# Performance work log

Measured on AMD Instinct MI355X. Metric: run time of the kernel, lower is better.

The kernel has to match this reference:

```python
import jax, jax.numpy as jnp
import numpy as np

KNOTS = 8
INTERVAL = 4.0
LAYERS = 8
WIDTH = 128
DX = 64
DY = 64
P = 3 * KNOTS - 1  # widths(K) + heights(K) + interior derivatives(K-1)
BATCH = 16384
MIN_DERIV = 1e-3
SOFTMAX_ADJ = 1e-2


def _made_masks(D, W):
    in_deg = np.arange(1, D + 1)
    hid_deg = (np.arange(W) % max(D - 1, 1)) + 1
    m1 = (hid_deg[:, None] >= in_deg[None, :]).astype(np.float32)        # (W, D)
    out_deg = np.repeat(np.arange(1, D + 1), P)                           # (D*P,)
    m2 = (out_deg[:, None] > hid_deg[None, :]).astype(np.float32)        # (D*P, W)
    return jnp.asarray(m1), jnp.asarray(m2)


def _adj_softmax(v):
    p = jax.nn.softmax(v, axis=-1)
    return (p + SOFTMAX_ADJ / v.shape[-1]) / (1.0 + SOFTMAX_ADJ)


def _rqs_transform(x, params):
    # x: (B, D); params: (B, D, P). Rational-quadratic spline on [-B_int, B_int], identity outside.
    Bi = INTERVAL
    w = params[..., :KNOTS]
    h = params[..., KNOTS:2 * KNOTS]
    d = params[..., 2 * KNOTS:]
    widths = _adj_softmax(w) * 2 * Bi
    heights = _adj_softmax(h) * 2 * Bi
    zero = jnp.zeros(x.shape + (1,), x.dtype)
    x_pos = -Bi + jnp.concatenate([zero, jnp.cumsum(widths, -1)], -1)   # (B, D, K+1)
    y_pos = -Bi + jnp.concatenate([zero, jnp.cumsum(heights, -1)], -1)
    derivs = jax.nn.softplus(d) + MIN_DERIV                              # (B, D, K-1)
    one = jnp.ones(x.shape + (1,), x.dtype)
    derivs = jnp.concatenate([one, derivs, one], -1)                     # (B, D, K+1), boundary derivs = 1
    inside = (x > -Bi) & (x < Bi)
    xc = jnp.clip(x, -Bi, Bi)
    # bin search (K is small; vectorized comparison)
    k = jnp.clip(jnp.sum((xc[..., None] >= x_pos), -1) - 1, 0, KNOTS - 1)

    def g(a, i):
        return jnp.take_along_axis(a, i[..., None], -1)[..., 0]

    xk, xk1 = g(x_pos, k), g(x_pos, k + 1)
    yk, yk1 = g(y_pos, k), g(y_pos, k + 1)
    dk, dk1 = g(derivs, k), g(derivs, k + 1)
    sk = (yk1 - yk) / (xk1 - xk)
    xi = (xc - xk) / (xk1 - xk)
    omx = 1.0 - xi
    den = sk + (dk1 + dk - 2.0 * sk) * xi * omx
    out = yk + (yk1 - yk) * (sk * xi * xi + dk * xi * omx) / den
    ld = 2.0 * jnp.log(sk) + jnp.log(dk1 * xi * xi + 2.0 * sk * xi * omx + dk * omx * omx) - 2.0 * jnp.log(den)
    return jnp.where(inside, out, x), jnp.where(inside, ld, 0.0)


def _maf_transform(x, W1, b1, Wout, bout, D):
    # Stacked layers: masked MLP -> elementwise RQ spline -> reverse permutation.
    m1, m2 = _made_masks(D, WIDTH)

    def layer(carry, ws):
        xc, ld = carry
        w1, bb1, wo, bo = ws
        hdn = jax.nn.relu(xc @ (w1 * m1).T + bb1)                # (B, W)
        p = (hdn @ (wo * m2).T + bo).reshape(xc.shape[0], D, P)  # (B, D, P)
        x2, ldj = _rqs_transform(xc, p)
        return (x2[:, ::-1], ld + ldj.sum(-1)), None

    init = (x, jnp.zeros(x.shape[0], x.dtype))
    (xf, ld), _ = jax.lax.scan(layer, init, (W1, b1, Wout, bout))
    return xf, ld


def setup_inputs() -> dict:
    key = jax.random.key(0)
    ks = jax.random.split(key, 10)
    s = 0.05
    return {
        "x": jax.random.normal(ks[0], (BATCH, DX), jnp.float32),
        "y": jax.random.normal(ks[1], (BATCH, DY), jnp.float32),
        "f_W1": jax.random.normal(ks[2], (LAYERS, WIDTH, DX), jnp.float32) * s,
        "f_b1": jnp.zeros((LAYERS, WIDTH), jnp.float32),
        "f_Wout": jax.random.normal(ks[3], (LAYERS, DX * P, WIDTH), jnp.float32) * s,
        "f_bout": jnp.zeros((LAYERS, DX * P), jnp.float32),
        "g_W1": jax.random.normal(ks[4], (LAYERS, WIDTH, DY), jnp.float32) * s,
        "g_b1": jnp.zeros((LAYERS, WIDTH), jnp.float32),
        "g_Wout": jax.random.normal(ks[5], (LAYERS, DY * P, WIDTH), jnp.float32) * s,
        "g_bout": jnp.zeros((LAYERS, DY * P), jnp.float32),
    }


def reference(x, y, f_W1, f_b1, f_Wout, f_bout, g_W1, g_b1, g_Wout, g_bout):
    xo, ldf = _maf_transform(x, f_W1, f_b1, f_Wout, f_bout, DX)
    yo, ldg = _maf_transform(y, g_W1, g_b1, g_Wout, g_bout, DY)
    return (xo, ldf, yo, ldg)
```

## Files before the change

kernel.cpp:

```cpp
#include <hip/hip_runtime.h>
#include <math.h>

#define BATCH   16384
#define DIMS    64
#define WID     128
#define KN      8
#define NP      23
#define NCOL    (DIMS * NP)
#define NLAYERS 8
#define BI_F    4.0f
#define GRP     92
#define NGRPB   8
#define LOG2E   1.44269504f

#define PF_WOUT (NLAYERS * NCOL * WID)
#define PF_W1   (NLAYERS * WID * DIMS)

typedef short s16x8 __attribute__((ext_vector_type(8)));
typedef float f32x4 __attribute__((ext_vector_type(4)));

__device__ __forceinline__ unsigned short f2bf(float f) {
    unsigned int u = __builtin_bit_cast(unsigned int, f);
    unsigned int r = (u + 0x7FFFu + ((u >> 16) & 1u)) >> 16;
    return (unsigned short)r;
}
__device__ __forceinline__ float bf2f(unsigned short u) {
    return __builtin_bit_cast(float, (unsigned int)u << 16);
}

__device__ __forceinline__ void stage16(const unsigned short* g, unsigned short* l) {
    __builtin_amdgcn_global_load_lds(
        (__attribute__((address_space(1))) void*)g,
        (__attribute__((address_space(3))) void*)l,
        16, 0, 0);
}

__global__ __launch_bounds__(256) void premask_kernel(
    const float* __restrict__ f_wout, const float* __restrict__ g_wout,
    const float* __restrict__ f_w1,   const float* __restrict__ g_w1,
    unsigned short* __restrict__ womask, unsigned short* __restrict__ w1mask,
    float* __restrict__ ldf, float* __restrict__ ldg)
{
    const int idx    = blockIdx.x * 256 + threadIdx.x;
    const int stride = gridDim.x * 256;

    const int totw = 2 * PF_WOUT;
    for (int i = idx; i < totw; i += stride) {
        int fl = i / PF_WOUT;
        int r  = i % PF_WOUT;
        int h  = r % WID;
        int o  = (r / WID) % NCOL;
        int d  = o / NP;
        int hd = h % (DIMS - 1) + 1;
        const float* src = fl ? g_wout : f_wout;
        unsigned short v = (hd <= d) ? f2bf(src[r] * LOG2E) : (unsigned short)0;
        const int dst = i - h + (h ^ ((o & 7) << 4));
        womask[dst] = v;
    }

    const int tot1 = 2 * PF_W1;
    for (int i = idx; i < tot1; i += stride) {
        int fl = i / PF_W1;
        int r  = i % PF_W1;
        int c  = r % DIMS;
        int w  = (r / DIMS) % WID;
        int deg = w % (DIMS - 1) + 1;
        const float* src = fl ? g_w1 : f_w1;
        w1mask[i] = (c < deg) ? f2bf(src[r]) : (unsigned short)0;
    }

    for (int i = idx; i < BATCH; i += stride) {
        ldf[i] = 0.0f;
        ldg[i] = 0.0f;
    }
}

__global__ __launch_bounds__(256)
__attribute__((amdgpu_waves_per_eu(4, 4)))
void layer_kernel(
    const float* __restrict__ xin_f, const float* __restrict__ xin_g,
    float* __restrict__ xout_f,      float* __restrict__ xout_g,
    const unsigned short* __restrict__ w1m_f, const unsigned short* __restrict__ w1m_g,
    const float* __restrict__ b1_f,  const float* __restrict__ b1_g,
    const unsigned short* __restrict__ wom_f, const unsigned short* __restrict__ wom_g,
    const float* __restrict__ bo_f,  const float* __restrict__ bo_g,
    float* __restrict__ ld_f,        float* __restrict__ ld_g)
{
    __shared__ __align__(16) unsigned short Wl[GRP * WID];
    __shared__ __align__(16) unsigned short S[4][2176];

    const int t     = threadIdx.x;
    const int wv    = t >> 6;
    const int ln    = t & 63;
    const int m     = ln & 15;
    const int q     = ln >> 4;
    const int flow  = blockIdx.y & 1;
    const int dhalf = blockIdx.y >> 1;
    const int g0    = dhalf * NGRPB;
    const int r0    = blockIdx.x * 64 + wv * 16;

    const float* xin          = flow ? xin_g : xin_f;
    float*       xout         = flow ? xout_g : xout_f;
    const unsigned short* w1m = flow ? w1m_g : w1m_f;
    const float* b1           = flow ? b1_g  : b1_f;
    const unsigned short* wom = flow ? wom_g : wom_f;
    const float* bo           = flow ? bo_g  : bo_f;
    float*       ldp          = flow ? ld_g  : ld_f;

    {
        const unsigned short* src = wom + (size_t)g0 * GRP * WID + ln * 8;
        #pragma unroll
        for (int i = 0; i < 6; ++i) {
            const int c = wv + 4 * i;
            if (c < 23) stage16(src + c * 512, Wl + c * 512);
        }
    }

    const float* xrow = xin + (size_t)(r0 + m) * DIMS;
    s16x8 xa[2];
    #pragma unroll
    for (int ks = 0; ks < 2; ++ks) {
        float4 v0 = *(const float4*)(xrow + ks * 32 + q * 8);
        float4 v1 = *(const float4*)(xrow + ks * 32 + q * 8 + 4);
        s16x8 a;
        a[0] = (short)f2bf(v0.x); a[1] = (short)f2bf(v0.y);
        a[2] = (short)f2bf(v0.z); a[3] = (short)f2bf(v0.w);
        a[4] = (short)f2bf(v1.x); a[5] = (short)f2bf(v1.y);
        a[6] = (short)f2bf(v1.z); a[7] = (short)f2bf(v1.w);
        xa[ks] = a;
    }

    f32x4 hacc[8];
    #pragma unroll
    for (int nt = 0; nt < 8; ++nt) {
        float bv = b1[nt * 16 + m];
        hacc[nt] = (f32x4){bv, bv, bv, bv};
    }
    #pragma unroll
    for (int ks = 0; ks < 2; ++ks) {
        #pragma unroll
        for (int nt = 0; nt < 8; ++nt) {
            s16x8 bfr = *(const s16x8*)(w1m + (nt * 16 + m) * DIMS + ks * 32 + q * 8);
            hacc[nt] = __builtin_amdgcn_mfma_f32_16x16x32_bf16(xa[ks], bfr, hacc[nt], 0, 0, 0);
        }
    }
    unsigned short* sw = &S[wv][0];
    #pragma unroll
    for (int nt = 0; nt < 8; ++nt) {
        #pragma unroll
        for (int rr = 0; rr < 4; ++rr) {
            sw[(q * 4 + rr) * 136 + nt * 16 + m] = f2bf(fmaxf(hacc[nt][rr], 0.0f));
        }
    }
    asm volatile("" ::: "memory");

    s16x8 af[4];
    #pragma unroll
    for (int ks = 0; ks < 4; ++ks)
        af[ks] = *(const s16x8*)&sw[m * 136 + ks * 32 + q * 8];
    asm volatile("" ::: "memory");

    float bnx[6];
    #pragma unroll
    for (int nt = 0; nt < 6; ++nt) {
        int o = g0 * GRP + nt * 16 + m;
        o = (o < NCOL) ? o : (NCOL - 1);
        bnx[nt] = bo[o] * LOG2E;
    }
    float xcur = xin[(size_t)(r0 + m) * DIMS + g0 * 4 + q];
    float xnxt = 0.0f;

    float ldsum = 0.0f;

    __syncthreads();

    #pragma unroll 1
    for (int gl = 0; gl < NGRPB; ++gl) {
        const int gg = g0 + gl;

        f32x4 acc[6];
        #pragma unroll
        for (int nt = 0; nt < 6; ++nt)
            acc[nt] = (f32x4){bnx[nt], bnx[nt], bnx[nt], bnx[nt]};

        const int swz = ((gg * 4 + m) & 7) << 4;
        #pragma unroll
        for (int ks = 0; ks < 4; ++ks) {
            #pragma unroll
            for (int nt = 0; nt < 6; ++nt) {
                const s16x8 bfr = *(const s16x8*)&Wl[
                    (nt * 16 + m) * WID + ((ks * 32 + q * 8) ^ swz)];
                acc[nt] = __builtin_amdgcn_mfma_f32_16x16x32_bf16(af[ks], bfr, acc[nt], 0, 0, 0);
            }
        }

        if (gl < NGRPB - 1) {
            __syncthreads();
            const unsigned short* src = wom + (size_t)(gg + 1) * GRP * WID + ln * 8;
            #pragma unroll
            for (int i = 0; i < 6; ++i) {
                const int c = wv + 4 * i;
                if (c < 23) stage16(src + c * 512, Wl + c * 512);
            }
            #pragma unroll
            for (int nt = 0; nt < 6; ++nt) {
                int o = (gg + 1) * GRP + nt * 16 + m;
                o = (o < NCOL) ? o : (NCOL - 1);
                bnx[nt] = bo[o] * LOG2E;
            }
            xnxt = xin[(size_t)(r0 + m) * DIMS + (gg + 1) * 4 + q];
        }

        #pragma unroll
        for (int nt = 0; nt < 6; ++nt) {
            const int c18 = (nt * 16 + m) * 18 + q * 4;
            #pragma unroll
            for (int rr = 0; rr < 4; ++rr)
                sw[c18 + rr] = f2bf(acc[nt][rr]);
        }

        {
            const int d = gg * 4 + q;

            float pp[NP];
            #pragma unroll
            for (int j = 0; j < NP; ++j)
                pp[j] = bf2f(sw[(q * 23 + j) * 18 + m]);

            const float xraw = xcur;

            float ew[KN], eh[KN];
            #pragma unroll
            for (int j = 0; j < KN; ++j) {
                ew[j] = exp2f(pp[j]);
                eh[j] = exp2f(pp[8 + j]);
            }
            const float sw_ = ((ew[0] + ew[1]) + (ew[2] + ew[3]))
                            + ((ew[4] + ew[5]) + (ew[6] + ew[7]));
            const float sh_ = ((eh[0] + eh[1]) + (eh[2] + eh[3]))
                            + ((eh[4] + eh[5]) + (eh[6] + eh[7]));
            const float cmul = 8.0f / 1.01f;
            const float cadd = 0.00125f * (8.0f / 1.01f);
            const float rw = cmul / sw_, rh = cmul / sh_;
            float width[KN], height[KN];
            #pragma unroll
            for (int j = 0; j < KN; ++j) {
                width[j]  = fmaf(ew[j], rw, cadd);
                height[j] = fmaf(eh[j], rh, cadd);
            }
            float dv[KN + 1];
            dv[0] = 1.0f; dv[KN] = 1.0f;
            #pragma unroll
            for (int i = 1; i < KN; ++i) {
                const float tt = exp2f(pp[15 + i]);
                dv[i] = fmaf(__log2f(1.0f + tt), 0.69314718f, 0.001f);
            }

            const bool inside = (xraw > -BI_F) && (xraw < BI_F);
            const float xcl = fminf(fmaxf(xraw, -BI_F), BI_F);

            float cx = -BI_F, cy = -BI_F;
            float xk = -BI_F, yk = -BI_F, xk1 = 0.f, yk1 = 0.f, dk = 1.f, dk1 = 1.f;
            #pragma unroll
            for (int i = 0; i < KN; ++i) {
                const float nx = cx + width[i];
                const float ny = cy + height[i];
                const bool cc = (xcl >= cx);
                xk  = cc ? cx : xk;    yk  = cc ? cy : yk;
                xk1 = cc ? nx : xk1;   yk1 = cc ? ny : yk1;
                dk  = cc ? dv[i] : dk; dk1 = cc ? dv[i + 1] : dk1;
                cx = nx; cy = ny;
            }

            const float invw = 1.0f / (xk1 - xk);
            const float sk   = (yk1 - yk) * invw;
            const float xi   = (xcl - xk) * invw;
            const float omx  = 1.0f - xi;
            const float den  = sk + (dk1 + dk - 2.0f * sk) * xi * omx;
            const float rden = 1.0f / den;
            float outv = fmaf((yk1 - yk) * (sk * xi * xi + dk * xi * omx), rden, yk);
            const float numl = dk1 * xi * xi + 2.0f * sk * xi * omx + dk * omx * omx;
            float ldj = __logf(sk * sk * numl * rden * rden);
            outv = inside ? outv : xraw;
            ldj  = inside ? ldj : 0.0f;

            xout[(size_t)(r0 + m) * DIMS + (DIMS - 1 - d)] = outv;
            ldsum += ldj;
        }

        if (gl < NGRPB - 1) {
            __syncthreads();
            xcur = xnxt;
        }
    }

    float v = ldsum + __shfl_xor(ldsum, 16, 64);
    v = v + __shfl_xor(v, 32, 64);
    if (ln < 16) {
        atomicAdd(ldp + (r0 + ln), v);
    }
}

extern "C" void kernel_launch(void* const* d_in, const int* in_sizes, int n_in,
                              void* d_out, int out_size, void* d_ws, size_t ws_size,
                              hipStream_t stream)
{
    const float* x      = (const float*)d_in[0];
    const float* y      = (const float*)d_in[1];
    const float* f_W1   = (const float*)d_in[2];
    const float* f_b1   = (const float*)d_in[3];
    const float* f_Wout = (const float*)d_in[4];
    const float* f_bout = (const float*)d_in[5];
    const float* g_W1   = (const float*)d_in[6];
    const float* g_b1   = (const float*)d_in[7];
    const float* g_Wout = (const float*)d_in[8];
    const float* g_bout = (const float*)d_in[9];

    float* out = (float*)d_out;
    float* xo  = out;
    float* ldf = out + (size_t)BATCH * DIMS;
    float* yo  = ldf + BATCH;
    float* ldg = yo + (size_t)BATCH * DIMS;

    unsigned short* womask = (unsigned short*)d_ws;
    unsigned short* w1mask = womask + 2 * (size_t)PF_WOUT;
    float* xA_f = (float*)(w1mask + 2 * (size_t)PF_W1);
    float* xA_g = xA_f + (size_t)BATCH * DIMS;

    premask_kernel<<<dim3(2048), dim3(256), 0, stream>>>(
        f_Wout, g_Wout, f_W1, g_W1, womask, w1mask, ldf, ldg);

    for (int l = 0; l < NLAYERS; ++l) {
        const float* inf = (l == 0) ? x : ((l & 1) ? xA_f : xo);
        const float* ing = (l == 0) ? y : ((l & 1) ? xA_g : yo);
        float* outf = (l & 1) ? xo : xA_f;
        float* outg = (l & 1) ? yo : xA_g;

        layer_kernel<<<dim3(BATCH / 64, 4), dim3(256), 0, stream>>>(
            inf, ing, outf, outg,
            w1mask + (size_t)l * WID * DIMS,
            w1mask + (size_t)PF_W1 + (size_t)l * WID * DIMS,
            f_b1 + (size_t)l * WID, g_b1 + (size_t)l * WID,
            womask + (size_t)l * NCOL * WID,
            womask + (size_t)PF_WOUT + (size_t)l * NCOL * WID,
            f_bout + (size_t)l * NCOL, g_bout + (size_t)l * NCOL,
            ldf, ldg);
    }
}
```

Before: 469.3 us.

## Fuse all eight flow layers into one persistent kernel with LDS-resident activations

Replaces the eight per-layer launches with a single kernel in which each block processes 64 rows through all layers. Activations are kept in double-buffered LDS instead of round-tripping through global memory, and the log-det is written once rather than accumulated with atomics. The grid drops from a 4-way split of output groups to a 2-way split across the flows, and occupancy is lowered to 2 waves/EU, so each block now streams all Wout groups itself. This removes launch overhead and intermediate traffic but reduces parallelism, with 512 blocks and longer serial work per block.

```diff
diff --git a/kernel.cpp b/kernel.cpp
--- a/kernel.cpp
+++ b/kernel.cpp
@@ -10,7 +10,8 @@
 #define NLAYERS 8
 #define BI_F    4.0f
 #define GRP     92
-#define NGRPB   8
+#define NGRP    16
+#define XPITCH  68
 #define LOG2E   1.44269504f
 
 #define PF_WOUT (NLAYERS * NCOL * WID)
@@ -38,8 +39,7 @@
 __global__ __launch_bounds__(256) void premask_kernel(
     const float* __restrict__ f_wout, const float* __restrict__ g_wout,
     const float* __restrict__ f_w1,   const float* __restrict__ g_w1,
-    unsigned short* __restrict__ womask, unsigned short* __restrict__ w1mask,
-    float* __restrict__ ldf, float* __restrict__ ldg)
+    unsigned short* __restrict__ womask, unsigned short* __restrict__ w1mask)
 {
     const int idx    = blockIdx.x * 256 + threadIdx.x;
     const int stride = gridDim.x * 256;
@@ -68,16 +68,11 @@
         const float* src = fl ? g_w1 : f_w1;
         w1mask[i] = (c < deg) ? f2bf(src[r]) : (unsigned short)0;
     }
-
-    for (int i = idx; i < BATCH; i += stride) {
-        ldf[i] = 0.0f;
-        ldg[i] = 0.0f;
-    }
 }
 
 __global__ __launch_bounds__(256)
-__attribute__((amdgpu_waves_per_eu(4, 4)))
-void layer_kernel(
+__attribute__((amdgpu_waves_per_eu(2, 2)))
+void flow8_kernel(
     const float* __restrict__ xin_f, const float* __restrict__ xin_g,
     float* __restrict__ xout_f,      float* __restrict__ xout_g,
     const unsigned short* __restrict__ w1m_f, const unsigned short* __restrict__ w1m_g,
@@ -88,16 +83,15 @@
 {
     __shared__ __align__(16) unsigned short Wl[GRP * WID];
     __shared__ __align__(16) unsigned short S[4][2176];
-
-    const int t     = threadIdx.x;
-    const int wv    = t >> 6;
-    const int ln    = t & 63;
-    const int m     = ln & 15;
-    const int q     = ln >> 4;
-    const int flow  = blockIdx.y & 1;
-    const int dhalf = blockIdx.y >> 1;
-    const int g0    = dhalf * NGRPB;
-    const int r0    = blockIdx.x * 64 + wv * 16;
+    __shared__ __align__(16) float Xf[2][4][16][XPITCH];
+
+    const int t    = threadIdx.x;
+    const int wv   = t >> 6;
+    const int ln   = t & 63;
+    const int m    = ln & 15;
+    const int q    = ln >> 4;
+    const int flow = blockIdx.y;
+    const int r0   = blockIdx.x * 64 + wv * 16;
 
     const float* xin          = flow ? xin_g : xin_f;
     float*       xout         = flow ? xout_g : xout_f;
@@ -108,7 +102,18 @@
     float*       ldp          = flow ? ld_g  : ld_f;
 
     {
-        const unsigned short* src = wom + (size_t)g0 * GRP * WID + ln * 8;
+        const int row = ln >> 2;
+        const int c0  = (ln & 3) * 16;
+        const float* srcr = xin + (size_t)(r0 + row) * DIMS + c0;
+        float* dstr = &Xf[0][wv][row][c0];
+        #pragma unroll
+        for (int i = 0; i < 4; ++i)
+            *(float4*)(dstr + i * 4) = *(const float4*)(srcr + i * 4);
+    }
+    asm volatile("" ::: "memory");
+
+    {
+        const unsigned short* src = wom + ln * 8;
         #pragma unroll
         for (int i = 0; i < 6; ++i) {
             const int c = wv + 4 * i;
@@ -116,188 +121,205 @@
         }
     }
 
-    const float* xrow = xin + (size_t)(r0 + m) * DIMS;
-    s16x8 xa[2];
-    #pragma unroll
-    for (int ks = 0; ks < 2; ++ks) {
-        float4 v0 = *(const float4*)(xrow + ks * 32 + q * 8);
-        float4 v1 = *(const float4*)(xrow + ks * 32 + q * 8 + 4);
-        s16x8 a;
-        a[0] = (short)f2bf(v0.x); a[1] = (short)f2bf(v0.y);
-        a[2] = (short)f2bf(v0.z); a[3] = (short)f2bf(v0.w);
-        a[4] = (short)f2bf(v1.x); a[5] = (short)f2bf(v1.y);
-        a[6] = (short)f2bf(v1.z); a[7] = (short)f2bf(v1.w);
-        xa[ks] = a;
-    }
-
-    f32x4 hacc[8];
-    #pragma unroll
-    for (int nt = 0; nt < 8; ++nt) {
-        float bv = b1[nt * 16 + m];
-        hacc[nt] = (f32x4){bv, bv, bv, bv};
-    }
-    #pragma unroll
-    for (int ks = 0; ks < 2; ++ks) {
-        #pragma unroll
-        for (int nt = 0; nt < 8; ++nt) {
-            s16x8 bfr = *(const s16x8*)(w1m + (nt * 16 + m) * DIMS + ks * 32 + q * 8);
-            hacc[nt] = __builtin_amdgcn_mfma_f32_16x16x32_bf16(xa[ks], bfr, hacc[nt], 0, 0, 0);
-        }
-    }
-    unsigned short* sw = &S[wv][0];
-    #pragma unroll
-    for (int nt = 0; nt < 8; ++nt) {
-        #pragma unroll
-        for (int rr = 0; rr < 4; ++rr) {
-            sw[(q * 4 + rr) * 136 + nt * 16 + m] = f2bf(fmaxf(hacc[nt][rr], 0.0f));
-        }
-    }
-    asm volatile("" ::: "memory");
-
-    s16x8 af[4];
-    #pragma unroll
-    for (int ks = 0; ks < 4; ++ks)
-        af[ks] = *(const s16x8*)&sw[m * 136 + ks * 32 + q * 8];
-    asm volatile("" ::: "memory");
-
     float bnx[6];
     #pragma unroll
-    for (int nt = 0; nt < 6; ++nt) {
-        int o = g0 * GRP + nt * 16 + m;
-        o = (o < NCOL) ? o : (NCOL - 1);
-        bnx[nt] = bo[o] * LOG2E;
-    }
-    float xcur = xin[(size_t)(r0 + m) * DIMS + g0 * 4 + q];
-    float xnxt = 0.0f;
+    for (int nt = 0; nt < 6; ++nt)
+        bnx[nt] = bo[nt * 16 + m] * LOG2E;
 
     float ldsum = 0.0f;
+    int cur = 0;
+    unsigned short* sw = &S[wv][0];
 
     __syncthreads();
 
     #pragma unroll 1
-    for (int gl = 0; gl < NGRPB; ++gl) {
-        const int gg = g0 + gl;
-
-        f32x4 acc[6];
-        #pragma unroll
-        for (int nt = 0; nt < 6; ++nt)
-            acc[nt] = (f32x4){bnx[nt], bnx[nt], bnx[nt], bnx[nt]};
-
-        const int swz = ((gg * 4 + m) & 7) << 4;
-        #pragma unroll
-        for (int ks = 0; ks < 4; ++ks) {
+    for (int l = 0; l < NLAYERS; ++l) {
+        const unsigned short* w1m_l = w1m + (size_t)l * WID * DIMS;
+        const float* b1_l           = b1 + (size_t)l * WID;
+        const int nxt = cur ^ 1;
+
+        s16x8 xa[2];
+        #pragma unroll
+        for (int ks = 0; ks < 2; ++ks) {
+            float4 v0 = *(const float4*)&Xf[cur][wv][m][ks * 32 + q * 8];
+            float4 v1 = *(const float4*)&Xf[cur][wv][m][ks * 32 + q * 8 + 4];
+            s16x8 a;
+            a[0] = (short)f2bf(v0.x); a[1] = (short)f2bf(v0.y);
+            a[2] = (short)f2bf(v0.z); a[3] = (short)f2bf(v0.w);
+            a[4] = (short)f2bf(v1.x); a[5] = (short)f2bf(v1.y);
+            a[6] = (short)f2bf(v1.z); a[7] = (short)f2bf(v1.w);
+            xa[ks] = a;
+        }
+
+        f32x4 hacc[8];
+        #pragma unroll
+        for (int nt = 0; nt < 8; ++nt) {
+            float bv = b1_l[nt * 16 + m];
+            hacc[nt] = (f32x4){bv, bv, bv, bv};
+        }
+        #pragma unroll
+        for (int ks = 0; ks < 2; ++ks) {
+            #pragma unroll
+            for (int nt = 0; nt < 8; ++nt) {
+                s16x8 bfr = *(const s16x8*)(w1m_l + (nt * 16 + m) * DIMS + ks * 32 + q * 8);
+                hacc[nt] = __builtin_amdgcn_mfma_f32_16x16x32_bf16(xa[ks], bfr, hacc[nt], 0, 0, 0);
+            }
+        }
+        #pragma unroll
+        for (int nt = 0; nt < 8; ++nt) {
+            #pragma unroll
+            for (int rr = 0; rr < 4; ++rr) {
+                sw[(q * 4 + rr) * 136 + nt * 16 + m] = f2bf(fmaxf(hacc[nt][rr], 0.0f));
+            }
+        }
+        asm volatile("" ::: "memory");
+
+        s16x8 af[4];
+        #pragma unroll
+        for (int ks = 0; ks < 4; ++ks)
+            af[ks] = *(const s16x8*)&sw[m * 136 + ks * 32 + q * 8];
+        asm volatile("" ::: "memory");
+
+        #pragma unroll 1
+        for (int g = 0; g < NGRP; ++g) {
+            const int gi = l * NGRP + g;
+
+            f32x4 acc[6];
+            #pragma unroll
+            for (int nt = 0; nt < 6; ++nt)
+                acc[nt] = (f32x4){bnx[nt], bnx[nt], bnx[nt], bnx[nt]};
+
+            const int swz = ((g * 4 + m) & 7) << 4;
+            #pragma unroll
+            for (int ks = 0; ks < 4; ++ks) {
+                #pragma unroll
+                for (int nt = 0; nt < 6; ++nt) {
+                    const s16x8 bfr = *(const s16x8*)&Wl[
+                        (nt * 16 + m) * WID + ((ks * 32 + q * 8) ^ swz)];
+                    acc[nt] = __builtin_amdgcn_mfma_f32_16x16x32_bf16(af[ks], bfr, acc[nt], 0, 0, 0);
+                }
+            }
+
+            if (gi < NLAYERS * NGRP - 1) {
+                __syncthreads();
+                const int l2 = (gi + 1) >> 4;
+                const int g2 = (gi + 1) & 15;
+                const unsigned short* src = wom +
+                    ((size_t)l2 * NCOL + (size_t)g2 * GRP) * WID + ln * 8;
+                #pragma unroll
+                for (int i = 0; i < 6; ++i) {
+                    const int c = wv + 4 * i;
+                    if (c < 23) stage16(src + c * 512, Wl + c * 512);
+                }
+                #pragma unroll
+                for (int nt = 0; nt < 6; ++nt) {
+                    int o = g2 * GRP + nt * 16 + m;
+                    o = (o < NCOL) ? o : (NCOL - 1);
+                    bnx[nt] = bo[(size_t)l2 * NCOL + o] * LOG2E;
+                }
+            }
+
             #pragma unroll
             for (int nt = 0; nt < 6; ++nt) {
-                const s16x8 bfr = *(const s16x8*)&Wl[
-                    (nt * 16 + m) * WID + ((ks * 32 + q * 8) ^ swz)];
-                acc[nt] = __builtin_amdgcn_mfma_f32_16x16x32_bf16(af[ks], bfr, acc[nt], 0, 0, 0);
-            }
-        }
-
-        if (gl < NGRPB - 1) {
-            __syncthreads();
-            const unsigned short* src = wom + (size_t)(gg + 1) * GRP * WID + ln * 8;
-            #pragma unroll
-            for (int i = 0; i < 6; ++i) {
-                const int c = wv + 4 * i;
-                if (c < 23) stage16(src + c * 512, Wl + c * 512);
-            }
-            #pragma unroll
-            for (int nt = 0; nt < 6; ++nt) {
-                int o = (gg + 1) * GRP + nt * 16 + m;
-                o = (o < NCOL) ? o : (NCOL - 1);
-                bnx[nt] = bo[o] * LOG2E;
-            }
-            xnxt = xin[(size_t)(r0 + m) * DIMS + (gg + 1) * 4 + q];
-        }
-
-        #pragma unroll
-        for (int nt = 0; nt < 6; ++nt) {
-            const int c18 = (nt * 16 + m) * 18 + q * 4;
-            #pragma unroll
-            for (int rr = 0; rr < 4; ++rr)
-                sw[c18 + rr] = f2bf(acc[nt][rr]);
-        }
-
-        {
-            const int d = gg * 4 + q;
-
-            float pp[NP];
-            #pragma unroll
-            for (int j = 0; j < NP; ++j)
-                pp[j] = bf2f(sw[(q * 23 + j) * 18 + m]);
-
-            const float xraw = xcur;
-
-            float ew[KN], eh[KN];
-            #pragma unroll
-            for (int j = 0; j < KN; ++j) {
-                ew[j] = exp2f(pp[j]);
-                eh[j] = exp2f(pp[8 + j]);
-            }
-            const float sw_ = ((ew[0] + ew[1]) + (ew[2] + ew[3]))
-                            + ((ew[4] + ew[5]) + (ew[6] + ew[7]));
-            const float sh_ = ((eh[0] + eh[1]) + (eh[2] + eh[3]))
-                            + ((eh[4] + eh[5]) + (eh[6] + eh[7]));
-            const float cmul = 8.0f / 1.01f;
-            const float cadd = 0.00125f * (8.0f / 1.01f);
-            const float rw = cmul / sw_, rh = cmul / sh_;
-            float width[KN], height[KN];
-            #pragma unroll
-            for (int j = 0; j < KN; ++j) {
-                width[j]  = fmaf(ew[j], rw, cadd);
-                height[j] = fmaf(eh[j], rh, cadd);
-            }
-            float dv[KN + 1];
-            dv[0] = 1.0f; dv[KN] = 1.0f;
-            #pragma unroll
-            for (int i = 1; i < KN; ++i) {
-                const float tt = exp2f(pp[15 + i]);
-                dv[i] = fmaf(__log2f(1.0f + tt), 0.69314718f, 0.001f);
-            }
-
-            const bool inside = (xraw > -BI_F) && (xraw < BI_F);
-            const float xcl = fminf(fmaxf(xraw, -BI_F), BI_F);
-
-            float cx = -BI_F, cy = -BI_F;
-            float xk = -BI_F, yk = -BI_F, xk1 = 0.f, yk1 = 0.f, dk = 1.f, dk1 = 1.f;
-            #pragma unroll
-            for (int i = 0; i < KN; ++i) {
-                const float nx = cx + width[i];
-                const float ny = cy + height[i];
-                const bool cc = (xcl >= cx);
-                xk  = cc ? cx : xk;    yk  = cc ? cy : yk;
-                xk1 = cc ? nx : xk1;   yk1 = cc ? ny : yk1;
-                dk  = cc ? dv[i] : dk; dk1 = cc ? dv[i + 1] : dk1;
-                cx = nx; cy = ny;
-            }
-
-            const float invw = 1.0f / (xk1 - xk);
-            const float sk   = (yk1 - yk) * invw;
-            const float xi   = (xcl - xk) * invw;
-            const float omx  = 1.0f - xi;
-            const float den  = sk + (dk1 + dk - 2.0f * sk) * xi * omx;
-            const float rden = 1.0f / den;
-            float outv = fmaf((yk1 - yk) * (sk * xi * xi + dk * xi * omx), rden, yk);
-            const float numl = dk1 * xi * xi + 2.0f * sk * xi * omx + dk * omx * omx;
-            float ldj = __logf(sk * sk * numl * rden * rden);
-            outv = inside ? outv : xraw;
-            ldj  = inside ? ldj : 0.0f;
-
-            xout[(size_t)(r0 + m) * DIMS + (DIMS - 1 - d)] = outv;
-            ldsum += ldj;
-        }
-
-        if (gl < NGRPB - 1) {
-            __syncthreads();
-            xcur = xnxt;
-        }
+                const int c18 = (nt * 16 + m) * 18 + q * 4;
+                #pragma unroll
+                for (int rr = 0; rr < 4; ++rr)
+                    sw[c18 + rr] = f2bf(acc[nt][rr]);
+            }
+
+            {
+                const int d = g * 4 + q;
+
+                float pp[NP];
+                #pragma unroll
+                for (int j = 0; j < NP; ++j)
+                    pp[j] = bf2f(sw[(q * 23 + j) * 18 + m]);
+
+                const float xraw = Xf[cur][wv][m][d];
+
+                float ew[KN], eh[KN];
+                #pragma unroll
+                for (int j = 0; j < KN; ++j) {
+                    ew[j] = exp2f(pp[j]);
+                    eh[j] = exp2f(pp[8 + j]);
+                }
+                const float sw_ = ((ew[0] + ew[1]) + (ew[2] + ew[3]))
+                                + ((ew[4] + ew[5]) + (ew[6] + ew[7]));
+                const float sh_ = ((eh[0] + eh[1]) + (eh[2] + eh[3]))
+                                + ((eh[4] + eh[5]) + (eh[6] + eh[7]));
+                const float cmul = 8.0f / 1.01f;
+                const float cadd = 0.00125f * (8.0f / 1.01f);
+                const float rw = cmul / sw_, rh = cmul / sh_;
+                float width[KN], height[KN];
+                #pragma unroll
+                for (int j = 0; j < KN; ++j) {
+                    width[j]  = fmaf(ew[j], rw, cadd);
+                    height[j] = fmaf(eh[j], rh, cadd);
+                }
+                float dv[KN + 1];
+                dv[0] = 1.0f; dv[KN] = 1.0f;
+                #pragma unroll
+                for (int i = 1; i < KN; ++i) {
+                    const float tt = exp2f(pp[15 + i]);
+                    dv[i] = fmaf(__log2f(1.0f + tt), 0.69314718f, 0.001f);
+                }
+
+                const bool inside = (xraw > -BI_F) && (xraw < BI_F);
+                const float xcl = fminf(fmaxf(xraw, -BI_F), BI_F);
+
+                float cx = -BI_F, cy = -BI_F;
+                float xk = -BI_F, yk = -BI_F, xk1 = 0.f, yk1 = 0.f, dk = 1.f, dk1 = 1.f;
+                #pragma unroll
+                for (int i = 0; i < KN; ++i) {
+                    const float nx = cx + width[i];
+                    const float ny = cy + height[i];
+                    const bool cc = (xcl >= cx);
+                    xk  = cc ? cx : xk;    yk  = cc ? cy : yk;
+                    xk1 = cc ? nx : xk1;   yk1 = cc ? ny : yk1;
+                    dk  = cc ? dv[i] : dk; dk1 = cc ? dv[i + 1] : dk1;
+                    cx = nx; cy = ny;
+                }
+
+                const float invw = 1.0f / (xk1 - xk);
+                const float sk   = (yk1 - yk) * invw;
+                const float xi   = (xcl - xk) * invw;
+                const float omx  = 1.0f - xi;
+                const float den  = sk + (dk1 + dk - 2.0f * sk) * xi * omx;
+                const float rden = 1.0f / den;
+                float outv = fmaf((yk1 - yk) * (sk * xi * xi + dk * xi * omx), rden, yk);
+                const float numl = dk1 * xi * xi + 2.0f * sk * xi * omx + dk * omx * omx;
+                float ldj = __logf(sk * sk * numl * rden * rden);
+                outv = inside ? outv : xraw;
+                ldj  = inside ? ldj : 0.0f;
+
+                Xf[nxt][wv][m][DIMS - 1 - d] = outv;
+                ldsum += ldj;
+            }
+
+            if (gi < NLAYERS * NGRP - 1) {
+                __syncthreads();
+            }
+        }
+
+        cur ^= 1;
+    }
+
+    asm volatile("" ::: "memory");
+
+    {
+        const int row = ln >> 2;
+        const int c0  = (ln & 3) * 16;
+        const float* srcr = &Xf[cur][wv][row][c0];
+        float* dstr = xout + (size_t)(r0 + row) * DIMS + c0;
+        #pragma unroll
+        for (int i = 0; i < 4; ++i)
+            *(float4*)(dstr + i * 4) = *(const float4*)(srcr + i * 4);
     }
 
     float v = ldsum + __shfl_xor(ldsum, 16, 64);
     v = v + __shfl_xor(v, 32, 64);
     if (ln < 16) {
-        atomicAdd(ldp + (r0 + ln), v);
+        ldp[r0 + ln] = v;
     }
 }
 
@@ -324,26 +346,15 @@
 
     unsigned short* womask = (unsigned short*)d_ws;
     unsigned short* w1mask = womask + 2 * (size_t)PF_WOUT;
-    float* xA_f = (float*)(w1mask + 2 * (size_t)PF_W1);
-    float* xA_g = xA_f + (size_t)BATCH * DIMS;
 
     premask_kernel<<<dim3(2048), dim3(256), 0, stream>>>(
-        f_Wout, g_Wout, f_W1, g_W1, womask, w1mask, ldf, ldg);
-
-    for (int l = 0; l < NLAYERS; ++l) {
-        const float* inf = (l == 0) ? x : ((l & 1) ? xA_f : xo);
-        const float* ing = (l == 0) ? y : ((l & 1) ? xA_g : yo);
-        float* outf = (l & 1) ? xo : xA_f;
-        float* outg = (l & 1) ? yo : xA_g;
-
-        layer_kernel<<<dim3(BATCH / 64, 4), dim3(256), 0, stream>>>(
-            inf, ing, outf, outg,
-            w1mask + (size_t)l * WID * DIMS,
-            w1mask + (size_t)PF_W1 + (size_t)l * WID * DIMS,
-            f_b1 + (size_t)l * WID, g_b1 + (size_t)l * WID,
-            womask + (size_t)l * NCOL * WID,
-            womask + (size_t)PF_WOUT + (size_t)l * NCOL * WID,
-            f_bout + (size_t)l * NCOL, g_bout + (size_t)l * NCOL,
-            ldf, ldg);
-    }
-}
+        f_Wout, g_Wout, f_W1, g_W1, womask, w1mask);
+
+    flow8_kernel<<<dim3(BATCH / 64, 2), dim3(256), 0, stream>>>(
+        x, y, xo, yo,
+        w1mask, w1mask + (size_t)PF_W1,
+        f_b1, g_b1,
+        womask, womask + (size_t)PF_WOUT,
+        f_bout, g_bout,
+        ldf, ldg);
+}
```

Result: faster. 453.9 us (-3.3%).
